# Optimization experiments

Hardware: AMD Instinct MI355X
Metric: run time of the kernel (lower is better)

## Reference

```python
import jax, jax.numpy as jnp
import numpy as np

B, S, E, H = 2, 2048, 2048, 16
D = E // H  # head_dim = 128
ROPE_BASE = 10000.0


def setup_inputs() -> dict:
    key = jax.random.key(0)
    ks = jax.random.split(key, 6)
    x = jax.random.normal(ks[0], (B, S, E), dtype=jnp.float32)
    # additive causal mask: 0 where attendable, -1e9 above diagonal
    causal = jnp.where(jnp.tril(jnp.ones((S, S), dtype=bool)), 0.0, -1e9).astype(jnp.float32)
    mask = jnp.broadcast_to(causal[None, None], (B, 1, S, S))
    # RoPE tables (rotate-half convention)
    inv_freq = 1.0 / (ROPE_BASE ** (jnp.arange(0, D, 2, dtype=jnp.float32) / D))
    freqs = jnp.arange(S, dtype=jnp.float32)[:, None] * inv_freq[None, :]  # [S, D/2]
    emb = jnp.concatenate([freqs, freqs], axis=-1)  # [S, D]
    cos, sin = jnp.cos(emb), jnp.sin(emb)
    std = 0.02
    Wq = jax.random.normal(ks[1], (E, E), dtype=jnp.float32) * std
    Wk = jax.random.normal(ks[2], (E, E), dtype=jnp.float32) * std
    Wv = jax.random.normal(ks[3], (E, E), dtype=jnp.float32) * std
    Wo = jax.random.normal(ks[4], (E, E), dtype=jnp.float32) * std
    zb = jnp.zeros((E,), dtype=jnp.float32)
    return {"x": x, "mask": mask, "cos": cos, "sin": sin,
            "Wq": Wq, "bq": zb, "Wk": Wk, "bk": zb, "Wv": Wv, "bv": zb,
            "Wo": Wo, "bo": zb, "rope_exclude": 0}


def _rotate_half(t):
    t1, t2 = jnp.split(t, 2, axis=-1)
    return jnp.concatenate([-t2, t1], axis=-1)


def _apply_rope(t, cos, sin, rope_exclude):
    # t: [B, H, S, D]; cos/sin: [S, D]
    rot = t * cos[None, None] + _rotate_half(t) * sin[None, None]
    keep = (jnp.arange(t.shape[2]) < rope_exclude)[None, None, :, None]
    return jnp.where(keep, t, rot)


def reference(x, mask, cos, sin, Wq, bq, Wk, bk, Wv, bv, Wo, bo, rope_exclude):
    b, s, e = x.shape
    scale = D ** -0.5
    def heads(y):
        return y.reshape(b, s, H, D).transpose(0, 2, 1, 3)  # [B,H,S,D]
    q = heads(x @ Wq.T + bq)
    k = heads(x @ Wk.T + bk)
    v = heads(x @ Wv.T + bv)
    q = _apply_rope(q, cos, sin, rope_exclude)
    k = _apply_rope(k, cos, sin, rope_exclude)
    scores = jnp.einsum('bhqd,bhkd->bhqk', q, k) * scale + mask
    attn = jax.nn.softmax(scores, axis=-1)  # dropout is identity in eval mode
    ctx = jnp.einsum('bhqk,bhkd->bhqd', attn, v)
    ctx = ctx.transpose(0, 2, 1, 3).reshape(b, s, e)
    return ctx @ Wo.T + bo
```

## Files before the change

### kernel.cpp

```cpp
#include <hip/hip_runtime.h>


#define BB 2
#define SS 2048
#define EE 2048
#define HH 16
#define DD 128
#define BH 32
#define MR 4096
#define BKK 64
#define NTK (EE / BKK)

typedef __attribute__((ext_vector_type(8))) short short8;
typedef __attribute__((ext_vector_type(4))) short short4v;
typedef __attribute__((ext_vector_type(4))) float floatx4;
typedef unsigned int u32;

__device__ __forceinline__ float bf2f(unsigned short u) {
    union { unsigned int i; float f; } v; v.i = ((unsigned int)u) << 16; return v.f;
}
__device__ __forceinline__ unsigned short f2bf(float f) {
    union { float f; unsigned int i; } v; v.f = f;
    unsigned int x = v.i;
    return (unsigned short)((x + 0x7fffu + ((x >> 16) & 1u)) >> 16);
}

__device__ __forceinline__ void async_copy16(const unsigned short* g, unsigned short* l) {
    __builtin_amdgcn_global_load_lds((const __attribute__((address_space(1))) u32*)g,
                                     (__attribute__((address_space(3))) u32*)l, 16, 0, 0);
}

__global__ __launch_bounds__(256)
void cvt_f32_bf16(const float* __restrict__ src, unsigned short* __restrict__ dst, int n)
{
    int i = (blockIdx.x * 256 + threadIdx.x) * 8;
    if (i < n) {
        floatx4 v0 = *(const floatx4*)&src[i];
        floatx4 v1 = *(const floatx4*)&src[i + 4];
        short8 o;
        #pragma unroll
        for (int j = 0; j < 4; ++j) { o[j] = (short)f2bf(v0[j]); o[4 + j] = (short)f2bf(v1[j]); }
        *(short8*)&dst[i] = o;
    }
}

__device__ __forceinline__ void stageA(const unsigned short* __restrict__ X,
                                       unsigned short* Asb, int mbase, int k0,
                                       int w, int lane)
{
    const int rsub = lane >> 3;
    const int ksw  = ((lane & 7) ^ rsub) << 3;
    #pragma unroll
    for (int h = 0; h < 2; ++h)
        #pragma unroll
        for (int c = 0; c < 2; ++c) {
            int r = h * 128 + (w * 2 + c) * 8 + rsub;
            async_copy16(&X[(size_t)(mbase + r) * EE + k0 + ksw],
                         &Asb[h * 8192 + (w * 2 + c) * 512]);
        }
}
__device__ __forceinline__ void stageB(const unsigned short* __restrict__ W,
                                       unsigned short* Bsb, int nbase, int k0,
                                       int w, int lane)
{
    const int rsub = lane >> 3;
    const int ksw  = ((lane & 7) ^ rsub) << 3;
    #pragma unroll
    for (int c = 0; c < 2; ++c) {
        int r = (w * 2 + c) * 8 + rsub;
        async_copy16(&W[(size_t)(nbase + r) * EE + k0 + ksw],
                     &Bsb[(w * 2 + c) * 512]);
    }
}

template<int MODE>
__global__ __launch_bounds__(512, 1)
void gemm8(const unsigned short* __restrict__ X,
           const unsigned short* __restrict__ W,
           const float* __restrict__ bias0,
           const float* __restrict__ bias1,
           const float* __restrict__ bias2,
           void* __restrict__ outv)
{
    __shared__ __align__(16) unsigned short As[3][256 * 64];
    __shared__ __align__(16) unsigned short Bs[3][128 * 64];

    const int NXB = (MODE == 0) ? 48 : 16;
    const int nwg = (MODE == 0) ? 768 : 256;
    const int q8  = nwg >> 3;
    const int wg  = ((int)blockIdx.x & 7) * q8 + ((int)blockIdx.x >> 3);
    const int xb = wg % NXB, yb = wg / NXB;
    const int mbase = yb * 256;
    const int nbase = xb * 128;

    const int tid  = threadIdx.x;
    const int w    = tid >> 6, lane = tid & 63;
    const int quad = lane >> 4, l16 = lane & 15;
    const int wm = w >> 1, wn = w & 1;

    floatx4 acc[4][4];
    #pragma unroll
    for (int mi = 0; mi < 4; ++mi)
        #pragma unroll
        for (int ni = 0; ni < 4; ++ni)
            acc[mi][ni] = (floatx4){0.f, 0.f, 0.f, 0.f};

    const int kx0 = (quad * 8) ^ ((l16 & 7) << 3);
    const int kx1 = (32 + quad * 8) ^ ((l16 & 7) << 3);

    stageA(X, As[0], mbase, 0,   w, lane);  stageB(W, Bs[0], nbase, 0,   w, lane);
    stageA(X, As[1], mbase, BKK, w, lane);  stageB(W, Bs[1], nbase, BKK, w, lane);
    asm volatile("s_waitcnt vmcnt(6)" ::: "memory");
    asm volatile("s_barrier" ::: "memory");

    for (int t = 0; t < NTK; ++t) {
        const unsigned short* Ab = As[t % 3];
        const unsigned short* Bb = Bs[t % 3];
        unsigned short* An = As[(t + 2) % 3];
        unsigned short* Bn = Bs[(t + 2) % 3];
        const bool pf = (t + 2 < NTK);
        const int kn = (t + 2) * BKK;

        short8 b[4][2];
        #pragma unroll
        for (int ni = 0; ni < 4; ++ni) {
            int rb = (wn * 64 + ni * 16 + l16) * 64;
            b[ni][0] = *(const short8*)&Bb[rb + kx0];
            b[ni][1] = *(const short8*)&Bb[rb + kx1];
        }
        short8 a[4][2];
        #pragma unroll
        for (int mi = 0; mi < 2; ++mi) {
            int ra = (wm * 64 + mi * 16 + l16) * 64;
            a[mi][0] = *(const short8*)&Ab[ra + kx0];
            a[mi][1] = *(const short8*)&Ab[ra + kx1];
        }
        if (pf) stageA(X, An, mbase, kn, w, lane);
        __builtin_amdgcn_s_setprio(1);
        #pragma unroll
        for (int mi = 0; mi < 2; ++mi)
            #pragma unroll
            for (int ni = 0; ni < 4; ++ni) {
                acc[mi][ni] = __builtin_amdgcn_mfma_f32_16x16x32_bf16(a[mi][0], b[ni][0], acc[mi][ni], 0, 0, 0);
                acc[mi][ni] = __builtin_amdgcn_mfma_f32_16x16x32_bf16(a[mi][1], b[ni][1], acc[mi][ni], 0, 0, 0);
            }
        __builtin_amdgcn_s_setprio(0);

        #pragma unroll
        for (int mi = 2; mi < 4; ++mi) {
            int ra = (wm * 64 + mi * 16 + l16) * 64;
            a[mi][0] = *(const short8*)&Ab[ra + kx0];
            a[mi][1] = *(const short8*)&Ab[ra + kx1];
        }
        if (pf) stageB(W, Bn, nbase, kn, w, lane);
        __builtin_amdgcn_s_setprio(1);
        #pragma unroll
        for (int mi = 2; mi < 4; ++mi)
            #pragma unroll
            for (int ni = 0; ni < 4; ++ni) {
                acc[mi][ni] = __builtin_amdgcn_mfma_f32_16x16x32_bf16(a[mi][0], b[ni][0], acc[mi][ni], 0, 0, 0);
                acc[mi][ni] = __builtin_amdgcn_mfma_f32_16x16x32_bf16(a[mi][1], b[ni][1], acc[mi][ni], 0, 0, 0);
            }
        __builtin_amdgcn_s_setprio(0);
        if (pf) asm volatile("s_waitcnt vmcnt(6)" ::: "memory");
        else    asm volatile("s_waitcnt vmcnt(0)" ::: "memory");
        asm volatile("s_barrier" ::: "memory");
    }

    #pragma unroll
    for (int ni = 0; ni < 4; ++ni) {
        int n = nbase + wn * 64 + ni * 16 + l16;
        float bval;
        if (MODE == 0) {
            const float* bp = (n < 2048) ? bias0 : (n < 4096) ? bias1 : bias2;
            bval = bp[n & (EE - 1)];
        } else {
            bval = bias0[n];
        }
        #pragma unroll
        for (int mi = 0; mi < 4; ++mi)
            #pragma unroll
            for (int rr = 0; rr < 4; ++rr) {
                int m = mbase + wm * 64 + mi * 16 + quad * 4 + rr;
                float val = acc[mi][ni][rr] + bval;
                if (MODE == 0) {
                    size_t idx = (size_t)(n >> 11) * ((size_t)BH * SS * DD)
                               + (((size_t)((m >> 11) * HH + ((n >> 7) & (HH - 1)))) * SS + (m & (SS - 1))) * DD
                               + (n & (DD - 1));
                    ((unsigned short*)outv)[idx] = f2bf(val);
                } else {
                    ((float*)outv)[(size_t)m * EE + n] = val;
                }
            }
    }
}

template<int MODE>
__global__ __launch_bounds__(256, 2)
void gemm_bt(const void* __restrict__ Xv,
             const float* __restrict__ W0,
             const float* __restrict__ W1,
             const float* __restrict__ W2,
             const float* __restrict__ bias0,
             const float* __restrict__ bias1,
             const float* __restrict__ bias2,
             void* __restrict__ outv)
{
    const float* W;
    const float* bias;
    unsigned short* op16 = nullptr;
    float* op32 = nullptr;
    if (MODE == 0) {
        int z = blockIdx.z;
        W    = (z == 0) ? W0 : (z == 1) ? W1 : W2;
        bias = (z == 0) ? bias0 : (z == 1) ? bias1 : bias2;
        op16 = (unsigned short*)outv + (size_t)z * ((size_t)BH * SS * DD);
    } else {
        W = W0; bias = bias0; op32 = (float*)outv;
    }

    __shared__ unsigned short As[4][128][8];
    __shared__ unsigned short Bs[4][128][8];

    const int tid  = threadIdx.x;
    const int wave = tid >> 6, lane = tid & 63;
    const int quad = lane >> 4, l16 = lane & 15;
    const int wr = (wave >> 1) * 64;
    const int wc = (wave & 1) * 64;
    const int mbase = blockIdx.y * 128, nbase = blockIdx.x * 128;

    const int srow  = tid >> 1;
    const int shalf = tid & 1;
    const int sc0   = shalf * 2;

    floatx4 acc[4][4];
    #pragma unroll
    for (int i = 0; i < 4; ++i)
        #pragma unroll
        for (int c = 0; c < 4; ++c)
            acc[i][c] = (floatx4){0.f, 0.f, 0.f, 0.f};

    const size_t arow = (size_t)(mbase + srow) * EE;
    const size_t brow = (size_t)(nbase + srow) * EE;

    for (int k0 = 0; k0 < EE; k0 += 32) {
        if (MODE == 0) {
            const float* px = &((const float*)Xv)[arow + k0 + shalf * 16];
            short8 lo, hi;
            #pragma unroll
            for (int j = 0; j < 8; ++j) lo[j] = (short)f2bf(px[j]);
            #pragma unroll
            for (int j = 0; j < 8; ++j) hi[j] = (short)f2bf(px[8 + j]);
            *(short8*)&As[sc0    ][srow][0] = lo;
            *(short8*)&As[sc0 + 1][srow][0] = hi;
        } else {
            const unsigned short* Xb = (const unsigned short*)Xv;
            *(short8*)&As[sc0    ][srow][0] = *(const short8*)&Xb[arow + k0 + shalf * 16];
            *(short8*)&As[sc0 + 1][srow][0] = *(const short8*)&Xb[arow + k0 + shalf * 16 + 8];
        }
        {
            const float* pw = &W[brow + k0 + shalf * 16];
            short8 lo, hi;
            #pragma unroll
            for (int j = 0; j < 8; ++j) lo[j] = (short)f2bf(pw[j]);
            #pragma unroll
            for (int j = 0; j < 8; ++j) hi[j] = (short)f2bf(pw[8 + j]);
            *(short8*)&Bs[sc0    ][srow][0] = lo;
            *(short8*)&Bs[sc0 + 1][srow][0] = hi;
        }
        __syncthreads();

        short8 a[4], b[4];
        #pragma unroll
        for (int i = 0; i < 4; ++i) a[i] = *(short8*)&As[quad][wr + i * 16 + l16][0];
        #pragma unroll
        for (int c = 0; c < 4; ++c) b[c] = *(short8*)&Bs[quad][wc + c * 16 + l16][0];
        #pragma unroll
        for (int i = 0; i < 4; ++i)
            #pragma unroll
            for (int c = 0; c < 4; ++c)
                acc[i][c] = __builtin_amdgcn_mfma_f32_16x16x32_bf16(a[i], b[c], acc[i][c], 0, 0, 0);
        __syncthreads();
    }

    #pragma unroll
    for (int c = 0; c < 4; ++c) {
        int n = nbase + wc + c * 16 + l16;
        float bval = bias[n];
        #pragma unroll
        for (int i = 0; i < 4; ++i) {
            #pragma unroll
            for (int r = 0; r < 4; ++r) {
                int m = mbase + wr + i * 16 + quad * 4 + r;
                float val = acc[i][c][r] + bval;
                if (MODE == 0) {
                    int bi = m >> 11, s = m & (SS - 1);
                    int h  = n >> 7,  d = n & (DD - 1);
                    op16[(((size_t)(bi * HH + h)) * SS + s) * DD + d] = f2bf(val);
                } else {
                    op32[(size_t)m * EE + n] = val;
                }
            }
        }
    }
}

__global__ __launch_bounds__(256)
void rope_kernel(unsigned short* __restrict__ Qw, unsigned short* __restrict__ Kw,
                 const float* __restrict__ cosT,
                 const float* __restrict__ sinT,
                 const int* __restrict__ rex)
{
    int idx = blockIdx.x * 256 + threadIdx.x;
    int d4 = idx & 15;
    int s  = (idx >> 4) & (SS - 1);
    int bh = (idx >> 15) & (BH - 1);
    int t  = idx >> 20;
    unsigned short* T = t ? Kw : Qw;
    const float qs = t ? 1.0f : 0.08838834764831845f;

    size_t base  = ((size_t)bh * SS + s) * DD + d4 * 4;
    size_t cbase = (size_t)s * DD + d4 * 4;

    short4v v1 = *(short4v*)&T[base];
    short4v v2 = *(short4v*)&T[base + 64];
    floatx4 c1 = *(const floatx4*)&cosT[cbase];
    floatx4 s1 = *(const floatx4*)&sinT[cbase];
    floatx4 c2 = *(const floatx4*)&cosT[cbase + 64];
    floatx4 s2 = *(const floatx4*)&sinT[cbase + 64];

    bool keep = (s < rex[0]);
    short4v o1, o2;
    #pragma unroll
    for (int i = 0; i < 4; ++i) {
        float f1 = bf2f((unsigned short)v1[i]);
        float f2 = bf2f((unsigned short)v2[i]);
        float r1 = f1 * c1[i] - f2 * s1[i];
        float r2 = f2 * c2[i] + f1 * s2[i];
        o1[i] = (short)f2bf((keep ? f1 : r1) * qs);
        o2[i] = (short)f2bf((keep ? f2 : r2) * qs);
    }
    *(short4v*)&T[base]      = o1;
    *(short4v*)&T[base + 64] = o2;
}

__global__ __launch_bounds__(256, 2)
void attn_mfma(const unsigned short* __restrict__ Qw,
               const unsigned short* __restrict__ Kw,
               const unsigned short* __restrict__ Vw,
               unsigned short* __restrict__ O)
{
    __shared__ unsigned short Ks[16][64][8];
    __shared__ unsigned short Vt[128][72];
    __shared__ unsigned short Ps[4][32][72];

    const int tid  = threadIdx.x;
    const int w    = tid >> 6, lane = tid & 63;
    const int quad = lane >> 4, l16 = lane & 15;
    const int bh = blockIdx.y;
    const int b = bh >> 4, h = bh & (HH - 1);
    const int qb = (bh < 16) ? ((SS / 128 - 1) - blockIdx.x) : blockIdx.x;
    const int qbase = qb * 128;

    const size_t head = (size_t)bh * SS * DD;

    short8 aq[2][4];
    #pragma unroll
    for (int hh = 0; hh < 2; ++hh) {
        const unsigned short* qp = &Qw[head + (size_t)(qbase + w * 32 + hh * 16 + l16) * DD];
        #pragma unroll
        for (int kc = 0; kc < 4; ++kc) aq[hh][kc] = *(const short8*)&qp[kc * 32 + quad * 8];
    }

    floatx4 oacc[2][8];
    #pragma unroll
    for (int hh = 0; hh < 2; ++hh)
        #pragma unroll
        for (int i = 0; i < 8; ++i) oacc[hh][i] = (floatx4){0.f, 0.f, 0.f, 0.f};
    float l_part[2][4];
    #pragma unroll
    for (int hh = 0; hh < 2; ++hh)
        #pragma unroll
        for (int r = 0; r < 4; ++r) l_part[hh][r] = 0.f;

    const int ntiles = 2 * qb + 2;
    for (int kt = 0; kt < ntiles; ++kt) {
        __syncthreads();

        #pragma unroll
        for (int it = 0; it < 4; ++it) {
            int key = it * 16 + (tid >> 4);
            int dc  = tid & 15;
            short8 v = *(const short8*)&Kw[head + (size_t)(kt * 64 + key) * DD + dc * 8];
            *(short8*)&Ks[dc][key ^ (dc & 7)][0] = v;
        }
        #pragma unroll
        for (int it = 0; it < 4; ++it) {
            int key = lane;
            int dc  = it * 4 + w;
            short8 v = *(const short8*)&Vw[head + (size_t)(kt * 64 + key) * DD + dc * 8];
            #pragma unroll
            for (int i = 0; i < 8; ++i) Vt[dc * 8 + i][key] = (unsigned short)v[i];
        }
        __syncthreads();

        if (kt * 64 > qbase + w * 32 + 31) continue;

        floatx4 sacc[2][4];
        #pragma unroll
        for (int hh = 0; hh < 2; ++hh)
            #pragma unroll
            for (int nt = 0; nt < 4; ++nt) sacc[hh][nt] = (floatx4){0.f, 0.f, 0.f, 0.f};
        #pragma unroll
        for (int kc = 0; kc < 4; ++kc) {
            int dcr = kc * 4 + quad;
            #pragma unroll
            for (int nt = 0; nt < 4; ++nt) {
                short8 bfrag = *(const short8*)&Ks[dcr][(nt * 16) + (l16 ^ (dcr & 7))][0];
                sacc[0][nt] = __builtin_amdgcn_mfma_f32_16x16x32_bf16(aq[0][kc], bfrag, sacc[0][nt], 0, 0, 0);
                sacc[1][nt] = __builtin_amdgcn_mfma_f32_16x16x32_bf16(aq[1][kc], bfrag, sacc[1][nt], 0, 0, 0);
            }
        }

        #pragma unroll
        for (int hh = 0; hh < 2; ++hh)
            #pragma unroll
            for (int nt = 0; nt < 4; ++nt)
                #pragma unroll
                for (int rr = 0; rr < 4; ++rr) {
                    int keyg = kt * 64 + nt * 16 + l16;
                    int qg   = qbase + w * 32 + hh * 16 + quad * 4 + rr;
                    float p = (keyg <= qg) ? __expf(sacc[hh][nt][rr]) : 0.f;
                    l_part[hh][rr] += p;
                    Ps[w][hh * 16 + quad * 4 + rr][nt * 16 + l16] = f2bf(p);
                }

        #pragma unroll
        for (int kc = 0; kc < 2; ++kc) {
            short8 pa0 = *(const short8*)&Ps[w][l16][kc * 32 + quad * 8];
            short8 pa1 = *(const short8*)&Ps[w][16 + l16][kc * 32 + quad * 8];
            #pragma unroll
            for (int nt = 0; nt < 8; ++nt) {
                short8 vb = *(const short8*)&Vt[nt * 16 + l16][kc * 32 + quad * 8];
                oacc[0][nt] = __builtin_amdgcn_mfma_f32_16x16x32_bf16(pa0, vb, oacc[0][nt], 0, 0, 0);
                oacc[1][nt] = __builtin_amdgcn_mfma_f32_16x16x32_bf16(pa1, vb, oacc[1][nt], 0, 0, 0);
            }
        }
    }

    #pragma unroll
    for (int hh = 0; hh < 2; ++hh)
        #pragma unroll
        for (int rr = 0; rr < 4; ++rr) {
            float l = l_part[hh][rr];
            l += __shfl_xor(l, 1, 16);
            l += __shfl_xor(l, 2, 16);
            l += __shfl_xor(l, 4, 16);
            l += __shfl_xor(l, 8, 16);
            float inv = 1.f / l;
            int qg = qbase + w * 32 + hh * 16 + quad * 4 + rr;
            unsigned short* cp = &O[((size_t)b * SS + qg) * EE + h * DD];
            #pragma unroll
            for (int nt = 0; nt < 8; ++nt)
                cp[nt * 16 + l16] = f2bf(oacc[hh][nt][rr] * inv);
        }
}

__global__ void sentinel_kernel(float* out, int n) {
    int i = blockIdx.x * 256 + threadIdx.x;
    if (i < n) out[i] = 1.0e6f;
}

extern "C" void kernel_launch(void* const* d_in, const int* in_sizes, int n_in,
                              void* d_out, int out_size, void* d_ws, size_t ws_size,
                              hipStream_t stream)
{
    const float* x    = (const float*)d_in[0];
    const float* cosT = (const float*)d_in[2];
    const float* sinT = (const float*)d_in[3];
    const float* Wq = (const float*)d_in[4];
    const float* bq = (const float*)d_in[5];
    const float* Wk = (const float*)d_in[6];
    const float* bk = (const float*)d_in[7];
    const float* Wv = (const float*)d_in[8];
    const float* bv = (const float*)d_in[9];
    const float* Wo = (const float*)d_in[10];
    const float* bo = (const float*)d_in[11];
    const int* rex = (const int*)d_in[12];

    const size_t tsz = (size_t)BH * SS * DD;
    const size_t wsz = (size_t)EE * EE;
    const size_t need_small = 4 * tsz * sizeof(unsigned short);
    const size_t need_big   = (3 * tsz + 4 * wsz + tsz) * sizeof(unsigned short);

    unsigned short* ws = (unsigned short*)d_ws;
    unsigned short* Qws = ws;
    unsigned short* Kws = ws + tsz;
    unsigned short* Vws = ws + 2 * tsz;

    if (ws_size >= need_big) {
        unsigned short* Wob = ws + 3 * tsz;
        unsigned short* Wqb = Wob + wsz;
        unsigned short* Wkb = Wqb + wsz;
        unsigned short* Wvb = Wkb + wsz;
        unsigned short* Xb  = Wvb + wsz;
        unsigned short* Cws = Xb;

        cvt_f32_bf16<<<(int)(tsz / 8 / 256), 256, 0, stream>>>(x,  Xb,  (int)tsz);
        cvt_f32_bf16<<<(int)(wsz / 8 / 256), 256, 0, stream>>>(Wq, Wqb, (int)wsz);
        cvt_f32_bf16<<<(int)(wsz / 8 / 256), 256, 0, stream>>>(Wk, Wkb, (int)wsz);
        cvt_f32_bf16<<<(int)(wsz / 8 / 256), 256, 0, stream>>>(Wv, Wvb, (int)wsz);
        cvt_f32_bf16<<<(int)(wsz / 8 / 256), 256, 0, stream>>>(Wo, Wob, (int)wsz);

        gemm8<0><<<768, 512, 0, stream>>>(Xb, Wqb, bq, bk, bv, Qws);
        rope_kernel<<<8192, 256, 0, stream>>>(Qws, Kws, cosT, sinT, rex);
        attn_mfma<<<dim3(SS / 128, BH), 256, 0, stream>>>(Qws, Kws, Vws, Cws);
        gemm8<1><<<256, 512, 0, stream>>>(Cws, Wob, bo, bo, bo, d_out);
    } else if (ws_size >= need_small) {
        unsigned short* Cws = ws + 3 * tsz;
        gemm_bt<0><<<dim3(16, 32, 3), 256, 0, stream>>>(x, Wq, Wk, Wv, bq, bk, bv, Qws);
        rope_kernel<<<8192, 256, 0, stream>>>(Qws, Kws, cosT, sinT, rex);
        attn_mfma<<<dim3(SS / 128, BH), 256, 0, stream>>>(Qws, Kws, Vws, Cws);
        gemm_bt<1><<<dim3(16, 32, 1), 256, 0, stream>>>(Cws, Wo, Wo, Wo, bo, bo, bo, d_out);
    } else {
        sentinel_kernel<<<(out_size + 255) / 256, 256, 0, stream>>>((float*)d_out, out_size);
    }
}
```

Baseline: 423.3 us.

## Fuse bf16 conversion launches and add intra-iteration barriers to GEMM main loop

```diff
diff --git a/kernel.cpp b/kernel.cpp
--- a/kernel.cpp
+++ b/kernel.cpp
@@ -31,17 +31,25 @@
 }
 
 __global__ __launch_bounds__(256)
-void cvt_f32_bf16(const float* __restrict__ src, unsigned short* __restrict__ dst, int n)
-{
-    int i = (blockIdx.x * 256 + threadIdx.x) * 8;
-    if (i < n) {
-        floatx4 v0 = *(const floatx4*)&src[i];
-        floatx4 v1 = *(const floatx4*)&src[i + 4];
-        short8 o;
-        #pragma unroll
-        for (int j = 0; j < 4; ++j) { o[j] = (short)f2bf(v0[j]); o[4 + j] = (short)f2bf(v1[j]); }
-        *(short8*)&dst[i] = o;
-    }
+void cvt_all(const float* __restrict__ x,  const float* __restrict__ Wq,
+             const float* __restrict__ Wk, const float* __restrict__ Wv,
+             const float* __restrict__ Wo, unsigned short* __restrict__ dst)
+{
+    const size_t wsz = (size_t)EE * EE;
+    size_t i = ((size_t)blockIdx.x * 256 + threadIdx.x) * 8;
+    const float* src; size_t off;
+    if      (i <     wsz) { src = Wo; off = 0; }
+    else if (i < 2 * wsz) { src = Wq; off = wsz; }
+    else if (i < 3 * wsz) { src = Wk; off = 2 * wsz; }
+    else if (i < 4 * wsz) { src = Wv; off = 3 * wsz; }
+    else                  { src = x;  off = 4 * wsz; }
+    const float* p = src + (i - off);
+    floatx4 v0 = *(const floatx4*)p;
+    floatx4 v1 = *(const floatx4*)(p + 4);
+    short8 o;
+    #pragma unroll
+    for (int j = 0; j < 4; ++j) { o[j] = (short)f2bf(v0[j]); o[4 + j] = (short)f2bf(v1[j]); }
+    *(short8*)&dst[i] = o;
 }
 
 __device__ __forceinline__ void stageA(const unsigned short* __restrict__ X,
@@ -111,7 +119,8 @@
     stageA(X, As[0], mbase, 0,   w, lane);  stageB(W, Bs[0], nbase, 0,   w, lane);
     stageA(X, As[1], mbase, BKK, w, lane);  stageB(W, Bs[1], nbase, BKK, w, lane);
     asm volatile("s_waitcnt vmcnt(6)" ::: "memory");
-    asm volatile("s_barrier" ::: "memory");
+    __builtin_amdgcn_s_barrier();
+    __builtin_amdgcn_sched_barrier(0);
 
     for (int t = 0; t < NTK; ++t) {
         const unsigned short* Ab = As[t % 3];
@@ -128,43 +137,55 @@
             b[ni][0] = *(const short8*)&Bb[rb + kx0];
             b[ni][1] = *(const short8*)&Bb[rb + kx1];
         }
-        short8 a[4][2];
+        short8 a0[2][2];
         #pragma unroll
         for (int mi = 0; mi < 2; ++mi) {
             int ra = (wm * 64 + mi * 16 + l16) * 64;
-            a[mi][0] = *(const short8*)&Ab[ra + kx0];
-            a[mi][1] = *(const short8*)&Ab[ra + kx1];
+            a0[mi][0] = *(const short8*)&Ab[ra + kx0];
+            a0[mi][1] = *(const short8*)&Ab[ra + kx1];
         }
         if (pf) stageA(X, An, mbase, kn, w, lane);
+        __builtin_amdgcn_sched_barrier(0);
+        __builtin_amdgcn_s_barrier();
+        __builtin_amdgcn_sched_barrier(0);
         __builtin_amdgcn_s_setprio(1);
         #pragma unroll
         for (int mi = 0; mi < 2; ++mi)
             #pragma unroll
             for (int ni = 0; ni < 4; ++ni) {
-                acc[mi][ni] = __builtin_amdgcn_mfma_f32_16x16x32_bf16(a[mi][0], b[ni][0], acc[mi][ni], 0, 0, 0);
-                acc[mi][ni] = __builtin_amdgcn_mfma_f32_16x16x32_bf16(a[mi][1], b[ni][1], acc[mi][ni], 0, 0, 0);
+                acc[mi][ni] = __builtin_amdgcn_mfma_f32_16x16x32_bf16(a0[mi][0], b[ni][0], acc[mi][ni], 0, 0, 0);
+                acc[mi][ni] = __builtin_amdgcn_mfma_f32_16x16x32_bf16(a0[mi][1], b[ni][1], acc[mi][ni], 0, 0, 0);
             }
         __builtin_amdgcn_s_setprio(0);
-
-        #pragma unroll
-        for (int mi = 2; mi < 4; ++mi) {
-            int ra = (wm * 64 + mi * 16 + l16) * 64;
-            a[mi][0] = *(const short8*)&Ab[ra + kx0];
-            a[mi][1] = *(const short8*)&Ab[ra + kx1];
+        __builtin_amdgcn_sched_barrier(0);
+        __builtin_amdgcn_s_barrier();
+        __builtin_amdgcn_sched_barrier(0);
+
+        short8 a1[2][2];
+        #pragma unroll
+        for (int mi = 0; mi < 2; ++mi) {
+            int ra = (wm * 64 + (2 + mi) * 16 + l16) * 64;
+            a1[mi][0] = *(const short8*)&Ab[ra + kx0];
+            a1[mi][1] = *(const short8*)&Ab[ra + kx1];
         }
         if (pf) stageB(W, Bn, nbase, kn, w, lane);
+        __builtin_amdgcn_sched_barrier(0);
+        __builtin_amdgcn_s_barrier();
+        __builtin_amdgcn_sched_barrier(0);
         __builtin_amdgcn_s_setprio(1);
         #pragma unroll
-        for (int mi = 2; mi < 4; ++mi)
+        for (int mi = 0; mi < 2; ++mi)
             #pragma unroll
             for (int ni = 0; ni < 4; ++ni) {
-                acc[mi][ni] = __builtin_amdgcn_mfma_f32_16x16x32_bf16(a[mi][0], b[ni][0], acc[mi][ni], 0, 0, 0);
-                acc[mi][ni] = __builtin_amdgcn_mfma_f32_16x16x32_bf16(a[mi][1], b[ni][1], acc[mi][ni], 0, 0, 0);
+                acc[2 + mi][ni] = __builtin_amdgcn_mfma_f32_16x16x32_bf16(a1[mi][0], b[ni][0], acc[2 + mi][ni], 0, 0, 0);
+                acc[2 + mi][ni] = __builtin_amdgcn_mfma_f32_16x16x32_bf16(a1[mi][1], b[ni][1], acc[2 + mi][ni], 0, 0, 0);
             }
         __builtin_amdgcn_s_setprio(0);
+        __builtin_amdgcn_sched_barrier(0);
         if (pf) asm volatile("s_waitcnt vmcnt(6)" ::: "memory");
         else    asm volatile("s_waitcnt vmcnt(0)" ::: "memory");
-        asm volatile("s_barrier" ::: "memory");
+        __builtin_amdgcn_s_barrier();
+        __builtin_amdgcn_sched_barrier(0);
     }
 
     #pragma unroll
@@ -506,11 +527,7 @@
         unsigned short* Xb  = Wvb + wsz;
         unsigned short* Cws = Xb;
 
-        cvt_f32_bf16<<<(int)(tsz / 8 / 256), 256, 0, stream>>>(x,  Xb,  (int)tsz);
-        cvt_f32_bf16<<<(int)(wsz / 8 / 256), 256, 0, stream>>>(Wq, Wqb, (int)wsz);
-        cvt_f32_bf16<<<(int)(wsz / 8 / 256), 256, 0, stream>>>(Wk, Wkb, (int)wsz);
-        cvt_f32_bf16<<<(int)(wsz / 8 / 256), 256, 0, stream>>>(Wv, Wvb, (int)wsz);
-        cvt_f32_bf16<<<(int)(wsz / 8 / 256), 256, 0, stream>>>(Wo, Wob, (int)wsz);
+        cvt_all<<<(int)((4 * wsz + tsz) / 8 / 256), 256, 0, stream>>>(x, Wq, Wk, Wv, Wo, Wob);
 
         gemm8<0><<<768, 512, 0, stream>>>(Xb, Wqb, bq, bk, bv, Qws);
         rope_kernel<<<8192, 256, 0, stream>>>(Qws, Kws, cosT, sinT, rex);
```

Result: slower. 431.8 us (+2.0%).

## Fuse RoPE and Q scaling into QKV GEMM epilogue; merge conversion launches

Applied to the files above, without the earlier changes.

```diff
diff --git a/kernel.cpp b/kernel.cpp
--- a/kernel.cpp
+++ b/kernel.cpp
@@ -31,17 +31,25 @@
 }
 
 __global__ __launch_bounds__(256)
-void cvt_f32_bf16(const float* __restrict__ src, unsigned short* __restrict__ dst, int n)
-{
-    int i = (blockIdx.x * 256 + threadIdx.x) * 8;
-    if (i < n) {
-        floatx4 v0 = *(const floatx4*)&src[i];
-        floatx4 v1 = *(const floatx4*)&src[i + 4];
-        short8 o;
-        #pragma unroll
-        for (int j = 0; j < 4; ++j) { o[j] = (short)f2bf(v0[j]); o[4 + j] = (short)f2bf(v1[j]); }
-        *(short8*)&dst[i] = o;
-    }
+void cvt_all(const float* __restrict__ x,  const float* __restrict__ Wq,
+             const float* __restrict__ Wk, const float* __restrict__ Wv,
+             const float* __restrict__ Wo, unsigned short* __restrict__ dst)
+{
+    const size_t wsz = (size_t)EE * EE;
+    size_t i = ((size_t)blockIdx.x * 256 + threadIdx.x) * 8;
+    const float* src; size_t off;
+    if      (i <     wsz) { src = Wo; off = 0; }
+    else if (i < 2 * wsz) { src = Wq; off = wsz; }
+    else if (i < 3 * wsz) { src = Wk; off = 2 * wsz; }
+    else if (i < 4 * wsz) { src = Wv; off = 3 * wsz; }
+    else                  { src = x;  off = 4 * wsz; }
+    const float* p = src + (i - off);
+    floatx4 v0 = *(const floatx4*)p;
+    floatx4 v1 = *(const floatx4*)(p + 4);
+    short8 o;
+    #pragma unroll
+    for (int j = 0; j < 4; ++j) { o[j] = (short)f2bf(v0[j]); o[4 + j] = (short)f2bf(v1[j]); }
+    *(short8*)&dst[i] = o;
 }
 
 __device__ __forceinline__ void stageA(const unsigned short* __restrict__ X,
@@ -80,6 +88,9 @@
            const float* __restrict__ bias0,
            const float* __restrict__ bias1,
            const float* __restrict__ bias2,
+           const float* __restrict__ cosT,
+           const float* __restrict__ sinT,
+           const int* __restrict__ rex,
            void* __restrict__ outv)
 {
     __shared__ __align__(16) unsigned short As[3][256 * 64];
@@ -167,31 +178,70 @@
         asm volatile("s_barrier" ::: "memory");
     }
 
-    #pragma unroll
-    for (int ni = 0; ni < 4; ++ni) {
-        int n = nbase + wn * 64 + ni * 16 + l16;
-        float bval;
-        if (MODE == 0) {
+    if (MODE == 1) {
+        #pragma unroll
+        for (int ni = 0; ni < 4; ++ni) {
+            int n = nbase + wn * 64 + ni * 16 + l16;
+            float bval = bias0[n];
+            #pragma unroll
+            for (int mi = 0; mi < 4; ++mi)
+                #pragma unroll
+                for (int rr = 0; rr < 4; ++rr) {
+                    int m = mbase + wm * 64 + mi * 16 + quad * 4 + rr;
+                    ((float*)outv)[(size_t)m * EE + n] = acc[mi][ni][rr] + bval;
+                }
+        }
+    } else {
+        unsigned short (*Ls)[132] = (unsigned short(*)[132])&As[0][0];
+        #pragma unroll
+        for (int ni = 0; ni < 4; ++ni) {
+            int nl = wn * 64 + ni * 16 + l16;
+            int n  = nbase + nl;
             const float* bp = (n < 2048) ? bias0 : (n < 4096) ? bias1 : bias2;
-            bval = bp[n & (EE - 1)];
-        } else {
-            bval = bias0[n];
-        }
-        #pragma unroll
-        for (int mi = 0; mi < 4; ++mi)
-            #pragma unroll
-            for (int rr = 0; rr < 4; ++rr) {
-                int m = mbase + wm * 64 + mi * 16 + quad * 4 + rr;
-                float val = acc[mi][ni][rr] + bval;
-                if (MODE == 0) {
-                    size_t idx = (size_t)(n >> 11) * ((size_t)BH * SS * DD)
-                               + (((size_t)((m >> 11) * HH + ((n >> 7) & (HH - 1)))) * SS + (m & (SS - 1))) * DD
-                               + (n & (DD - 1));
-                    ((unsigned short*)outv)[idx] = f2bf(val);
-                } else {
-                    ((float*)outv)[(size_t)m * EE + n] = val;
-                }
+            float bval = bp[n & (EE - 1)];
+            #pragma unroll
+            for (int mi = 0; mi < 4; ++mi)
+                #pragma unroll
+                for (int rr = 0; rr < 4; ++rr)
+                    Ls[wm * 64 + mi * 16 + quad * 4 + rr][nl] = f2bf(acc[mi][ni][rr] + bval);
+        }
+        __syncthreads();
+
+        const int r0 = tid >> 4;
+        const int c0 = (tid & 15) * 4;
+        const int nz = nbase + c0;
+        const int z  = nz >> 11;
+        const int hh = (nz >> 7) & (HH - 1);
+        const float qs = (z == 0) ? 0.08838834764831845f : 1.0f;
+        const int rexv = rex[0];
+        unsigned short* op16 = (unsigned short*)outv;
+        #pragma unroll
+        for (int rr2 = 0; rr2 < 8; ++rr2) {
+            int row = r0 * 8 + rr2;
+            int m = mbase + row;
+            int s = m & (SS - 1), bi = m >> 11;
+            short4v lo = *(short4v*)&Ls[row][c0];
+            short4v hi = *(short4v*)&Ls[row][c0 + 64];
+            floatx4 c1 = *(const floatx4*)&cosT[(size_t)s * DD + c0];
+            floatx4 s1 = *(const floatx4*)&sinT[(size_t)s * DD + c0];
+            floatx4 c2 = *(const floatx4*)&cosT[(size_t)s * DD + c0 + 64];
+            floatx4 s2 = *(const floatx4*)&sinT[(size_t)s * DD + c0 + 64];
+            bool rot = (z < 2) && (s >= rexv);
+            short4v o1, o2;
+            #pragma unroll
+            for (int c = 0; c < 4; ++c) {
+                float f1 = bf2f((unsigned short)lo[c]);
+                float f2 = bf2f((unsigned short)hi[c]);
+                float r1 = rot ? (f1 * c1[c] - f2 * s1[c]) : f1;
+                float r2 = rot ? (f2 * c2[c] + f1 * s2[c]) : f2;
+                o1[c] = (short)f2bf(r1 * qs);
+                o2[c] = (short)f2bf(r2 * qs);
             }
+            size_t base = (size_t)z * ((size_t)BH * SS * DD)
+                        + ((size_t)(bi * HH + hh) * SS + s) * DD;
+            *(short4v*)&op16[base + c0]      = o1;
+            *(short4v*)&op16[base + c0 + 64] = o2;
+        }
     }
 }
 
@@ -506,16 +556,11 @@
         unsigned short* Xb  = Wvb + wsz;
         unsigned short* Cws = Xb;
 
-        cvt_f32_bf16<<<(int)(tsz / 8 / 256), 256, 0, stream>>>(x,  Xb,  (int)tsz);
-        cvt_f32_bf16<<<(int)(wsz / 8 / 256), 256, 0, stream>>>(Wq, Wqb, (int)wsz);
-        cvt_f32_bf16<<<(int)(wsz / 8 / 256), 256, 0, stream>>>(Wk, Wkb, (int)wsz);
-        cvt_f32_bf16<<<(int)(wsz / 8 / 256), 256, 0, stream>>>(Wv, Wvb, (int)wsz);
-        cvt_f32_bf16<<<(int)(wsz / 8 / 256), 256, 0, stream>>>(Wo, Wob, (int)wsz);
-
-        gemm8<0><<<768, 512, 0, stream>>>(Xb, Wqb, bq, bk, bv, Qws);
-        rope_kernel<<<8192, 256, 0, stream>>>(Qws, Kws, cosT, sinT, rex);
+        cvt_all<<<(int)((4 * wsz + tsz) / 8 / 256), 256, 0, stream>>>(x, Wq, Wk, Wv, Wo, Wob);
+
+        gemm8<0><<<768, 512, 0, stream>>>(Xb, Wqb, bq, bk, bv, cosT, sinT, rex, Qws);
         attn_mfma<<<dim3(SS / 128, BH), 256, 0, stream>>>(Qws, Kws, Vws, Cws);
-        gemm8<1><<<256, 512, 0, stream>>>(Cws, Wob, bo, bo, bo, d_out);
+        gemm8<1><<<256, 512, 0, stream>>>(Cws, Wob, bo, bo, bo, cosT, sinT, rex, d_out);
     } else if (ws_size >= need_small) {
         unsigned short* Cws = ws + 3 * tsz;
         gemm_bt<0><<<dim3(16, 32, 3), 256, 0, stream>>>(x, Wq, Wk, Wv, bq, bk, bv, Qws);
```

Measured after the change: 414.8 us. -2.0%, faster.
